# Kernel optimization log

Hardware: AMD Instinct MI355X
Metric: run time of the kernel (lower is better)

## Reference

```python
import jax, jax.numpy as jnp
import numpy as np

N_ENT, N_REL, E_DIM, R_DIM, K, B = 100000, 64, 128, 128, 32, 16384


def _lookup_maxnorm(table, ids):
    # torch nn.Embedding(max_norm=1): rows with L2 norm > 1 are renormed to 1 at lookup
    x = table[ids]
    n = jnp.linalg.norm(x, axis=-1, keepdims=True)
    return x * jnp.minimum(1.0, 1.0 / jnp.maximum(n, 1e-12))


def setup_inputs() -> dict:
    key = jax.random.key(0)
    ks = jax.random.split(key, 10)
    xavier = lambda k, shp: jax.random.uniform(k, shp, jnp.float32, -1.0, 1.0) * np.sqrt(6.0 / (shp[0] + shp[1]))
    return {
        "idx": jax.random.randint(ks[0], (B,), 0, N_ENT),
        "adj_ent": jax.random.randint(ks[1], (N_ENT, K), 0, N_ENT),
        "adj_rel": jax.random.randint(ks[2], (N_ENT, K), 0, N_REL),
        "ent_table": xavier(ks[3], (N_ENT, E_DIM)),
        "rel_table": xavier(ks[4], (N_REL, R_DIM)),
        "Wr_w": xavier(ks[5], (R_DIM, E_DIM)),
        "Wr_b": jnp.zeros((R_DIM,), jnp.float32),
        "W1_w": xavier(ks[6], (E_DIM, E_DIM)),
        "W1_b": jnp.zeros((E_DIM,), jnp.float32),
        "W2_w": xavier(ks[7], (E_DIM, E_DIM)),
        "W2_b": jnp.zeros((E_DIM,), jnp.float32),
    }


def reference(idx, adj_ent, adj_rel, ent_table, rel_table, Wr_w, Wr_b, W1_w, W1_b, W2_w, W2_b):
    idx = jnp.clip(idx, 0, N_ENT - 1)
    e_ids = adj_ent[idx]                      # [B, K]
    r_ids = adj_rel[idx]                      # [B, K]
    t = _lookup_maxnorm(ent_table, e_ids)     # [B, K, E]
    r = _lookup_maxnorm(rel_table, r_ids)     # [B, K, R]
    h = _lookup_maxnorm(ent_table, idx)       # [B, E]
    # GAT message pass
    hr = h @ Wr_w.T + Wr_b                    # [B, R]
    tr = t @ Wr_w.T + Wr_b                    # [B, K, R]
    score = jnp.sum(jnp.tanh(hr[:, None, :] + r) * tr, axis=-1, keepdims=True)  # [B, K, 1]
    att = jax.nn.softmax(score, axis=1)
    Nh = jnp.sum(t * att, axis=1)             # [B, E]
    # Bi-Interaction aggregate
    leaky = lambda x: jax.nn.leaky_relu(x, 0.2)
    return leaky((h + Nh) @ W1_w.T + W1_b) + leaky((h * Nh) @ W2_w.T + W2_b)
```

## Files before the change

kernel.cpp:

```cpp
#include <hip/hip_runtime.h>
#include <hip/hip_fp16.h>
#include <math.h>

#define N_ENT 100000
#define N_REL 64
#define DIM   128
#define KNB   32
#define BATCH 16384

typedef _Float16 f16;
typedef __attribute__((ext_vector_type(8))) _Float16 f16x8;
typedef __attribute__((ext_vector_type(4))) _Float16 f16x4;
typedef __attribute__((ext_vector_type(4))) float floatx4;

__device__ __forceinline__ int clamp_id(int id) {
    return id < 0 ? 0 : (id > N_ENT - 1 ? N_ENT - 1 : id);
}

__device__ __forceinline__ float poly_tanh(float x) {
    const float x2 = x * x;
    return x * fmaf(x2, fmaf(x2, 0.13333334f, -0.33333334f), 1.0f);
}

__global__ __launch_bounds__(256) void k_small(
    const float* __restrict__ Wr, const float* __restrict__ W1,
    const float* __restrict__ W2, f16* __restrict__ Wr16,
    f16* __restrict__ W116, f16* __restrict__ W216,
    const float* __restrict__ rel, __half2* __restrict__ REL2)
{
    if (blockIdx.x < 64) {
        const int t = blockIdx.x * 256 + threadIdx.x;
        Wr16[t] = (f16)Wr[t];
        W116[t] = (f16)W1[t];
        W216[t] = (f16)W2[t];
    } else {
        const int lane = threadIdx.x & 63;
        const int row  = (blockIdx.x - 64) * 4 + (threadIdx.x >> 6);
        const float2 x = *(const float2*)(rel + row * DIM + 2 * lane);
        float ss = x.x * x.x + x.y * x.y;
        #pragma unroll
        for (int m = 1; m < 64; m <<= 1) ss += __shfl_xor(ss, m);
        const float s = fminf(1.0f, 1.0f / fmaxf(sqrtf(ss), 1e-12f));
        REL2[row * 64 + lane] = __floats2half2_rn(x.x * s, x.y * s);
    }
}

__global__ __launch_bounds__(256, 4) void k_pre(
    const float* __restrict__ ent, const f16* __restrict__ B,
    const float* __restrict__ bias, f16* __restrict__ C16)
{
    const int wid  = threadIdx.x >> 6;
    const int lane = threadIdx.x & 63;
    const int ds = blockIdx.x * 4 + wid;
    if (ds >= N_ENT / 32) return;
    const int row0 = ds * 32;
    const int mm = lane & 15, quad = lane >> 4;

    const float* __restrict__ src0 = ent + (size_t)(row0 + mm) * DIM + quad * 8;
    const float* __restrict__ src1 = src0 + 16 * DIM;

    float x0[4][8], x1[4][8];
    #pragma unroll
    for (int kt = 0; kt < 4; ++kt) {
        *(float4*)&x0[kt][0] = *(const float4*)(src0 + kt * 32);
        *(float4*)&x0[kt][4] = *(const float4*)(src0 + kt * 32 + 4);
        *(float4*)&x1[kt][0] = *(const float4*)(src1 + kt * 32);
        *(float4*)&x1[kt][4] = *(const float4*)(src1 + kt * 32 + 4);
    }

    float ss0 = 0.0f, ss1 = 0.0f;
    #pragma unroll
    for (int kt = 0; kt < 4; ++kt)
        #pragma unroll
        for (int j = 0; j < 8; ++j) {
            ss0 = fmaf(x0[kt][j], x0[kt][j], ss0);
            ss1 = fmaf(x1[kt][j], x1[kt][j], ss1);
        }
    ss0 += __shfl_xor(ss0, 16); ss0 += __shfl_xor(ss0, 32);
    ss1 += __shfl_xor(ss1, 16); ss1 += __shfl_xor(ss1, 32);
    const float s0 = fminf(1.0f, 1.0f / fmaxf(sqrtf(ss0), 1e-12f));
    const float s1 = fminf(1.0f, 1.0f / fmaxf(sqrtf(ss1), 1e-12f));

    f16* __restrict__ n0 = C16 + (size_t)(row0 + mm) * 256 + 128 + quad * 8;
    f16* __restrict__ n1 = n0 + 16 * 256;
    f16x8 a0[4], a1[4];
    #pragma unroll
    for (int kt = 0; kt < 4; ++kt) {
        f16x8 v0, v1;
        #pragma unroll
        for (int j = 0; j < 8; ++j) {
            v0[j] = (f16)(x0[kt][j] * s0);
            v1[j] = (f16)(x1[kt][j] * s1);
        }
        a0[kt] = v0; a1[kt] = v1;
        *(f16x8*)(n0 + kt * 32) = v0;
        *(f16x8*)(n1 + kt * 32) = v1;
    }

    f16* __restrict__ t0 = C16 + (size_t)(row0 + mm) * 256;
    f16* __restrict__ t1 = t0 + 16 * 256;
    #pragma unroll
    for (int ct = 0; ct < 8; ++ct) {
        f16x8 w[4];
        #pragma unroll
        for (int kt = 0; kt < 4; ++kt)
            w[kt] = *(const f16x8*)(B + (size_t)(ct * 16 + mm) * DIM + kt * 32 + quad * 8);
        floatx4 acc0 = {0.0f, 0.0f, 0.0f, 0.0f};
        floatx4 acc1 = {0.0f, 0.0f, 0.0f, 0.0f};
        #pragma unroll
        for (int kt = 0; kt < 4; ++kt) {
            acc0 = __builtin_amdgcn_mfma_f32_16x16x32_f16(w[kt], a0[kt], acc0, 0, 0, 0);
            acc1 = __builtin_amdgcn_mfma_f32_16x16x32_f16(w[kt], a1[kt], acc1, 0, 0, 0);
        }
        const float4 bb = *(const float4*)(bias + ct * 16 + quad * 4);
        f16x4 o0, o1;
        #pragma unroll
        for (int r = 0; r < 4; ++r) {
            o0[r] = (f16)(acc0[r] + ((const float*)&bb)[r]);
            o1[r] = (f16)(acc1[r] + ((const float*)&bb)[r]);
        }
        *(f16x4*)(t0 + ct * 16 + quad * 4) = o0;
        *(f16x4*)(t1 + ct * 16 + quad * 4) = o1;
    }
}

__global__ __launch_bounds__(256, 4) void k_sa(
    const int* __restrict__ idx, const int* __restrict__ adj_ent,
    const int* __restrict__ adj_rel, const unsigned int* __restrict__ C32,
    const __half2* __restrict__ REL2,
    __half2* __restrict__ U2, __half2* __restrict__ V2)
{
    const int wid  = threadIdx.x >> 6;
    const int lane = threadIdx.x & 63;
    const int b = blockIdx.x * 4 + wid;

    const int id = clamp_id(idx[b]);
    const unsigned int hr_u = C32[(size_t)id * 128 + lane];
    const unsigned int h_u  = C32[(size_t)id * 128 + 64 + lane];
    const int eL = adj_ent[(size_t)id * KNB + (lane & 31)];
    const int rL = adj_rel[(size_t)id * KNB + (lane & 31)];

    unsigned int trd[KNB], tnd[KNB];
    #pragma unroll
    for (int k = 0; k < KNB; ++k) {
        const int e = __builtin_amdgcn_readlane(eL, k);
        const unsigned int* __restrict__ rowp = C32 + (size_t)e * 128 + lane;
        trd[k] = rowp[0];
        tnd[k] = rowp[64];
    }

    const float2 hr = __half22float2(*(const __half2*)&hr_u);
    float p[KNB];
    #pragma unroll
    for (int k = 0; k < KNB; ++k) {
        const int r = __builtin_amdgcn_readlane(rL, k);
        const float2 tr = __half22float2(*(const __half2*)&trd[k]);
        const float2 rn = __half22float2(REL2[r * 64 + lane]);
        p[k] = poly_tanh(hr.x + rn.x) * tr.x + poly_tanh(hr.y + rn.y) * tr.y;
    }

    #pragma unroll
    for (int step = 0; step < 5; ++step) {
        const int half = 16 >> step;
        const int mask = 1 << step;
        const bool hi_lane = (lane & mask) != 0;
        #pragma unroll
        for (int i = 0; i < 16; ++i) {
            if (i >= half) break;
            const float lo = p[i], hi = p[i + half];
            const float send = hi_lane ? lo : hi;
            const float recv = __shfl_xor(send, mask);
            p[i] = (hi_lane ? hi : lo) + recv;
        }
    }
    const float sc = p[0] + __shfl_xor(p[0], 32);

    const float ex = __expf(sc);
    float tt = ex;
    #pragma unroll
    for (int m = 1; m < 32; m <<= 1) tt += __shfl_xor(tt, m);
    const float attL = ex * __builtin_amdgcn_rcpf(tt);

    float nh0 = 0.0f, nh1 = 0.0f;
    #pragma unroll
    for (int k = 0; k < KNB; ++k) {
        const float a = __uint_as_float(
            __builtin_amdgcn_readlane(__float_as_uint(attL), k));
        const float2 t = __half22float2(*(const __half2*)&tnd[k]);
        nh0 = fmaf(a, t.x, nh0);
        nh1 = fmaf(a, t.y, nh1);
    }

    const float2 h = __half22float2(*(const __half2*)&h_u);
    U2[(size_t)b * 64 + lane] = __floats2half2_rn(h.x + nh0, h.y + nh1);
    V2[(size_t)b * 64 + lane] = __floats2half2_rn(h.x * nh0, h.y * nh1);
}

__global__ __launch_bounds__(256, 4) void k_gemm_out(
    const f16* __restrict__ U, const f16* __restrict__ V,
    const f16* __restrict__ W1h, const float* __restrict__ b1,
    const f16* __restrict__ W2h, const float* __restrict__ b2,
    float* __restrict__ out)
{
    const int wid  = threadIdx.x >> 6;
    const int lane = threadIdx.x & 63;
    const int g = blockIdx.x * 4 + wid;
    const int strip = g >> 2;
    const int ct0 = (g & 3) * 2;
    const int row0 = strip * 16;
    const int mm = lane & 15, quad = lane >> 4;

    f16x8 au[4], av[4];
    #pragma unroll
    for (int kt = 0; kt < 4; ++kt) {
        au[kt] = *(const f16x8*)(U + (size_t)(row0 + mm) * DIM + kt * 32 + quad * 8);
        av[kt] = *(const f16x8*)(V + (size_t)(row0 + mm) * DIM + kt * 32 + quad * 8);
    }

    #pragma unroll
    for (int c = 0; c < 2; ++c) {
        const int ct = ct0 + c;
        floatx4 accU = {0.0f, 0.0f, 0.0f, 0.0f};
        floatx4 accV = {0.0f, 0.0f, 0.0f, 0.0f};
        #pragma unroll
        for (int kt = 0; kt < 4; ++kt) {
            const f16x8 wu = *(const f16x8*)(W1h + (size_t)(ct * 16 + mm) * DIM + kt * 32 + quad * 8);
            const f16x8 wv = *(const f16x8*)(W2h + (size_t)(ct * 16 + mm) * DIM + kt * 32 + quad * 8);
            accU = __builtin_amdgcn_mfma_f32_16x16x32_f16(wu, au[kt], accU, 0, 0, 0);
            accV = __builtin_amdgcn_mfma_f32_16x16x32_f16(wv, av[kt], accV, 0, 0, 0);
        }
        const float4 bb1 = *(const float4*)(b1 + ct * 16 + quad * 4);
        const float4 bb2 = *(const float4*)(b2 + ct * 16 + quad * 4);
        float4 o;
        #pragma unroll
        for (int r = 0; r < 4; ++r) {
            const float xv = accU[r] + ((const float*)&bb1)[r];
            const float yv = accV[r] + ((const float*)&bb2)[r];
            const float lx = xv > 0.0f ? xv : 0.2f * xv;
            const float ly = yv > 0.0f ? yv : 0.2f * yv;
            ((float*)&o)[r] = lx + ly;
        }
        *(float4*)(out + (size_t)(row0 + mm) * DIM + ct * 16 + quad * 4) = o;
    }
}

extern "C" void kernel_launch(void* const* d_in, const int* in_sizes, int n_in,
                              void* d_out, int out_size, void* d_ws, size_t ws_size,
                              hipStream_t stream) {
    (void)in_sizes; (void)n_in; (void)out_size; (void)ws_size;
    const int*   idx     = (const int*)d_in[0];
    const int*   adj_ent = (const int*)d_in[1];
    const int*   adj_rel = (const int*)d_in[2];
    const float* ent     = (const float*)d_in[3];
    const float* rel     = (const float*)d_in[4];
    const float* Wr_w    = (const float*)d_in[5];
    const float* Wr_b    = (const float*)d_in[6];
    const float* W1_w    = (const float*)d_in[7];
    const float* W1_b    = (const float*)d_in[8];
    const float* W2_w    = (const float*)d_in[9];
    const float* W2_b    = (const float*)d_in[10];
    float* out = (float*)d_out;

    char* ws = (char*)d_ws;
    f16* C16   = (f16*)(ws);
    f16* REL16 = (f16*)(ws + 51200000);
    f16* U16   = (f16*)(ws + 51216384);
    f16* V16   = (f16*)(ws + 55410688);
    f16* Wr16  = (f16*)(ws + 59604992);
    f16* W116  = (f16*)(ws + 59637760);
    f16* W216  = (f16*)(ws + 59670528);

    k_small<<<dim3(80), dim3(256), 0, stream>>>(Wr_w, W1_w, W2_w, Wr16, W116, W216,
                                                rel, (__half2*)REL16);
    k_pre<<<dim3((N_ENT / 32 + 3) / 4), dim3(256), 0, stream>>>(ent, Wr16, Wr_b, C16);
    k_sa<<<dim3(BATCH / 4), dim3(256), 0, stream>>>(idx, adj_ent, adj_rel,
                                                    (const unsigned int*)C16,
                                                    (const __half2*)REL16,
                                                    (__half2*)U16, (__half2*)V16);
    k_gemm_out<<<dim3(1024), dim3(256), 0, stream>>>(U16, V16, W116, W1_b,
                                                     W216, W2_b, out);
}
```

Baseline: 206.3 us.

## Stage entity rows and neighbor gathers through LDS via direct global-to-LDS loads

k_pre becomes a persistent kernel: each wave processes 16-row strips and double-buffers the fp32 entity rows into LDS with global_load_lds, using an XOR swizzle to avoid bank conflicts, so the next strip's load overlaps the current strip's normalization and MFMA. k_sa now gathers the 32 neighbor rows straight into LDS with 4-byte global_load_lds instead of holding 64 values per lane in registers, which lowers register pressure. The cost is 64KB of shared memory per block in both kernels, so launch bounds drop to 2 blocks per CU, which cuts occupancy and with it the latency hiding on the gather-bound path.

```diff
diff --git a/kernel.cpp b/kernel.cpp
--- a/kernel.cpp
+++ b/kernel.cpp
@@ -7,6 +7,7 @@
 #define DIM   128
 #define KNB   32
 #define BATCH 16384
+#define STRIPS (N_ENT / 16)
 
 typedef _Float16 f16;
 typedef __attribute__((ext_vector_type(8))) _Float16 f16x8;
@@ -21,6 +22,18 @@
     const float x2 = x * x;
     return x * fmaf(x2, fmaf(x2, 0.13333334f, -0.33333334f), 1.0f);
 }
+
+__device__ __forceinline__ void dma16(const void* g, void* l) {
+    __builtin_amdgcn_global_load_lds(
+        (const __attribute__((address_space(1))) unsigned int*)g,
+        (__attribute__((address_space(3))) unsigned int*)l, 16, 0, 0);
+}
+__device__ __forceinline__ void dma4(const void* g, void* l) {
+    __builtin_amdgcn_global_load_lds(
+        (const __attribute__((address_space(1))) unsigned int*)g,
+        (__attribute__((address_space(3))) unsigned int*)l, 4, 0, 0);
+}
+#define WAIT_VM0() __builtin_amdgcn_s_waitcnt(0x0F70)
 
 __global__ __launch_bounds__(256) void k_small(
     const float* __restrict__ Wr, const float* __restrict__ W1,
@@ -45,116 +58,132 @@
     }
 }
 
-__global__ __launch_bounds__(256, 4) void k_pre(
+__global__ __launch_bounds__(256, 2) void k_pre(
     const float* __restrict__ ent, const f16* __restrict__ B,
     const float* __restrict__ bias, f16* __restrict__ C16)
 {
+    __shared__ float xs[4][2][16 * DIM];
     const int wid  = threadIdx.x >> 6;
     const int lane = threadIdx.x & 63;
-    const int ds = blockIdx.x * 4 + wid;
-    if (ds >= N_ENT / 32) return;
-    const int row0 = ds * 32;
     const int mm = lane & 15, quad = lane >> 4;
-
-    const float* __restrict__ src0 = ent + (size_t)(row0 + mm) * DIM + quad * 8;
-    const float* __restrict__ src1 = src0 + 16 * DIM;
-
-    float x0[4][8], x1[4][8];
-    #pragma unroll
-    for (int kt = 0; kt < 4; ++kt) {
-        *(float4*)&x0[kt][0] = *(const float4*)(src0 + kt * 32);
-        *(float4*)&x0[kt][4] = *(const float4*)(src0 + kt * 32 + 4);
-        *(float4*)&x1[kt][0] = *(const float4*)(src1 + kt * 32);
-        *(float4*)&x1[kt][4] = *(const float4*)(src1 + kt * 32 + 4);
-    }
-
-    float ss0 = 0.0f, ss1 = 0.0f;
-    #pragma unroll
-    for (int kt = 0; kt < 4; ++kt)
-        #pragma unroll
-        for (int j = 0; j < 8; ++j) {
-            ss0 = fmaf(x0[kt][j], x0[kt][j], ss0);
-            ss1 = fmaf(x1[kt][j], x1[kt][j], ss1);
-        }
-    ss0 += __shfl_xor(ss0, 16); ss0 += __shfl_xor(ss0, 32);
-    ss1 += __shfl_xor(ss1, 16); ss1 += __shfl_xor(ss1, 32);
-    const float s0 = fminf(1.0f, 1.0f / fmaxf(sqrtf(ss0), 1e-12f));
-    const float s1 = fminf(1.0f, 1.0f / fmaxf(sqrtf(ss1), 1e-12f));
-
-    f16* __restrict__ n0 = C16 + (size_t)(row0 + mm) * 256 + 128 + quad * 8;
-    f16* __restrict__ n1 = n0 + 16 * 256;
-    f16x8 a0[4], a1[4];
-    #pragma unroll
-    for (int kt = 0; kt < 4; ++kt) {
-        f16x8 v0, v1;
-        #pragma unroll
-        for (int j = 0; j < 8; ++j) {
-            v0[j] = (f16)(x0[kt][j] * s0);
-            v1[j] = (f16)(x1[kt][j] * s1);
-        }
-        a0[kt] = v0; a1[kt] = v1;
-        *(f16x8*)(n0 + kt * 32) = v0;
-        *(f16x8*)(n1 + kt * 32) = v1;
-    }
-
-    f16* __restrict__ t0 = C16 + (size_t)(row0 + mm) * 256;
-    f16* __restrict__ t1 = t0 + 16 * 256;
-    #pragma unroll
-    for (int ct = 0; ct < 8; ++ct) {
-        f16x8 w[4];
+    const int gw = blockIdx.x * 4 + wid;
+    const int NW = gridDim.x * 4;
+
+    float* const buf0 = &xs[wid][0][0];
+    float* const buf1 = &xs[wid][1][0];
+
+    if (gw < STRIPS) {
+        const char* gb = (const char*)ent + (size_t)gw * 8192;
+        #pragma unroll
+        for (int k = 0; k < 8; ++k) {
+            const int lu = k * 64 + lane;
+            const int gu = lu ^ ((lu >> 5) & 7);
+            dma16(gb + (size_t)gu * 16, (char*)buf0 + (size_t)k * 1024);
+        }
+    }
+
+    int parity = 0;
+    for (int s = gw; s < STRIPS; s += NW) {
+        WAIT_VM0();
+        const float* __restrict__ cur = parity ? buf1 : buf0;
+
+        float x[4][8];
+        #pragma unroll
+        for (int kt = 0; kt < 4; ++kt) {
+            const int u0 = mm * 32 + kt * 8 + quad * 2;
+            const int f0 = (u0 ^ (mm & 7)) * 4;
+            const int f1 = ((u0 + 1) ^ (mm & 7)) * 4;
+            *(float4*)&x[kt][0] = *(const float4*)(cur + f0);
+            *(float4*)&x[kt][4] = *(const float4*)(cur + f1);
+        }
+
+        const int sn = s + NW;
+        if (sn < STRIPS) {
+            const char* gb = (const char*)ent + (size_t)sn * 8192;
+            char* nb = (char*)(parity ? buf0 : buf1);
+            #pragma unroll
+            for (int k = 0; k < 8; ++k) {
+                const int lu = k * 64 + lane;
+                const int gu = lu ^ ((lu >> 5) & 7);
+                dma16(gb + (size_t)gu * 16, nb + (size_t)k * 1024);
+            }
+        }
+        parity ^= 1;
+
+        float ss = 0.0f;
         #pragma unroll
         for (int kt = 0; kt < 4; ++kt)
-            w[kt] = *(const f16x8*)(B + (size_t)(ct * 16 + mm) * DIM + kt * 32 + quad * 8);
-        floatx4 acc0 = {0.0f, 0.0f, 0.0f, 0.0f};
-        floatx4 acc1 = {0.0f, 0.0f, 0.0f, 0.0f};
+            #pragma unroll
+            for (int j = 0; j < 8; ++j) ss = fmaf(x[kt][j], x[kt][j], ss);
+        ss += __shfl_xor(ss, 16);
+        ss += __shfl_xor(ss, 32);
+        const float sc = fminf(1.0f, 1.0f / fmaxf(sqrtf(ss), 1e-12f));
+
+        const int row0 = s * 16;
+        f16* __restrict__ n0 = C16 + (size_t)(row0 + mm) * 256 + 128 + quad * 8;
+        f16x8 a[4];
         #pragma unroll
         for (int kt = 0; kt < 4; ++kt) {
-            acc0 = __builtin_amdgcn_mfma_f32_16x16x32_f16(w[kt], a0[kt], acc0, 0, 0, 0);
-            acc1 = __builtin_amdgcn_mfma_f32_16x16x32_f16(w[kt], a1[kt], acc1, 0, 0, 0);
-        }
-        const float4 bb = *(const float4*)(bias + ct * 16 + quad * 4);
-        f16x4 o0, o1;
-        #pragma unroll
-        for (int r = 0; r < 4; ++r) {
-            o0[r] = (f16)(acc0[r] + ((const float*)&bb)[r]);
-            o1[r] = (f16)(acc1[r] + ((const float*)&bb)[r]);
-        }
-        *(f16x4*)(t0 + ct * 16 + quad * 4) = o0;
-        *(f16x4*)(t1 + ct * 16 + quad * 4) = o1;
-    }
-}
-
-__global__ __launch_bounds__(256, 4) void k_sa(
+            f16x8 v;
+            #pragma unroll
+            for (int j = 0; j < 8; ++j) v[j] = (f16)(x[kt][j] * sc);
+            a[kt] = v;
+            *(f16x8*)(n0 + kt * 32) = v;
+        }
+
+        f16* __restrict__ t0 = C16 + (size_t)(row0 + mm) * 256;
+        #pragma unroll
+        for (int ct = 0; ct < 8; ++ct) {
+            floatx4 acc = {0.0f, 0.0f, 0.0f, 0.0f};
+            #pragma unroll
+            for (int kt = 0; kt < 4; ++kt) {
+                const f16x8 w = *(const f16x8*)(B + (size_t)(ct * 16 + mm) * DIM + kt * 32 + quad * 8);
+                acc = __builtin_amdgcn_mfma_f32_16x16x32_f16(w, a[kt], acc, 0, 0, 0);
+            }
+            const float4 bb = *(const float4*)(bias + ct * 16 + quad * 4);
+            f16x4 o;
+            #pragma unroll
+            for (int r = 0; r < 4; ++r)
+                o[r] = (f16)(acc[r] + ((const float*)&bb)[r]);
+            *(f16x4*)(t0 + ct * 16 + quad * 4) = o;
+        }
+    }
+}
+
+__global__ __launch_bounds__(256, 2) void k_sa(
     const int* __restrict__ idx, const int* __restrict__ adj_ent,
     const int* __restrict__ adj_rel, const unsigned int* __restrict__ C32,
     const __half2* __restrict__ REL2,
     __half2* __restrict__ U2, __half2* __restrict__ V2)
 {
+    __shared__ unsigned int sn[4][KNB * 128];
     const int wid  = threadIdx.x >> 6;
     const int lane = threadIdx.x & 63;
     const int b = blockIdx.x * 4 + wid;
 
     const int id = clamp_id(idx[b]);
+    const int eL = adj_ent[(size_t)id * KNB + (lane & 31)];
+    const int rL = adj_rel[(size_t)id * KNB + (lane & 31)];
+    unsigned int* const lbase = &sn[wid][0];
+
+    #pragma unroll
+    for (int k = 0; k < KNB; ++k) {
+        const int e = __builtin_amdgcn_readlane(eL, k);
+        const unsigned int* g = C32 + (size_t)e * 128 + lane;
+        dma4(g,      lbase + k * 128);
+        dma4(g + 64, lbase + k * 128 + 64);
+    }
     const unsigned int hr_u = C32[(size_t)id * 128 + lane];
     const unsigned int h_u  = C32[(size_t)id * 128 + 64 + lane];
-    const int eL = adj_ent[(size_t)id * KNB + (lane & 31)];
-    const int rL = adj_rel[(size_t)id * KNB + (lane & 31)];
-
-    unsigned int trd[KNB], tnd[KNB];
-    #pragma unroll
-    for (int k = 0; k < KNB; ++k) {
-        const int e = __builtin_amdgcn_readlane(eL, k);
-        const unsigned int* __restrict__ rowp = C32 + (size_t)e * 128 + lane;
-        trd[k] = rowp[0];
-        tnd[k] = rowp[64];
-    }
+    WAIT_VM0();
 
     const float2 hr = __half22float2(*(const __half2*)&hr_u);
     float p[KNB];
     #pragma unroll
     for (int k = 0; k < KNB; ++k) {
         const int r = __builtin_amdgcn_readlane(rL, k);
-        const float2 tr = __half22float2(*(const __half2*)&trd[k]);
+        const unsigned int trd = lbase[k * 128 + lane];
+        const float2 tr = __half22float2(*(const __half2*)&trd);
         const float2 rn = __half22float2(REL2[r * 64 + lane]);
         p[k] = poly_tanh(hr.x + rn.x) * tr.x + poly_tanh(hr.y + rn.y) * tr.y;
     }
@@ -186,7 +215,8 @@
     for (int k = 0; k < KNB; ++k) {
         const float a = __uint_as_float(
             __builtin_amdgcn_readlane(__float_as_uint(attL), k));
-        const float2 t = __half22float2(*(const __half2*)&tnd[k]);
+        const unsigned int tnd = lbase[k * 128 + 64 + lane];
+        const float2 t = __half22float2(*(const __half2*)&tnd);
         nh0 = fmaf(a, t.x, nh0);
         nh1 = fmaf(a, t.y, nh1);
     }
@@ -272,7 +302,7 @@
 
     k_small<<<dim3(80), dim3(256), 0, stream>>>(Wr_w, W1_w, W2_w, Wr16, W116, W216,
                                                 rel, (__half2*)REL16);
-    k_pre<<<dim3((N_ENT / 32 + 3) / 4), dim3(256), 0, stream>>>(ent, Wr16, Wr_b, C16);
+    k_pre<<<dim3(521), dim3(256), 0, stream>>>(ent, Wr16, Wr_b, C16);
     k_sa<<<dim3(BATCH / 4), dim3(256), 0, stream>>>(idx, adj_ent, adj_rel,
                                                     (const unsigned int*)C16,
                                                     (const __half2*)REL16,
```

Measured after the change: 216.0 us. +4.7%, slower.
